# Kernel tuning notes

Hardware: AMD Instinct MI355X
Metric: run time of the kernel (lower is better)

Reference implementation:

```python
import jax, jax.numpy as jnp
import numpy as np

HIDDEN = 2048
HEADS = 16
HEAD_DIM = HIDDEN // HEADS  # 128
ROPE_BASE = 10000.0


def _rope_cos_sin(seq_len, head_dim, dtype):
    inv_freq = 1.0 / (ROPE_BASE ** (jnp.arange(0, head_dim, 2, dtype=jnp.float32) / head_dim))
    pos = jnp.arange(seq_len, dtype=jnp.float32)
    freqs = pos[:, None] * inv_freq[None, :]            # [S, D/2]
    emb = jnp.concatenate([freqs, freqs], axis=-1)      # [S, D]
    return jnp.cos(emb).astype(dtype), jnp.sin(emb).astype(dtype)


def _rotate_half(x):
    x1, x2 = jnp.split(x, 2, axis=-1)
    return jnp.concatenate([-x2, x1], axis=-1)


def apply_rope(q, k, seq_len):
    # q, k: [B, H, S, Dh]
    cos, sin = _rope_cos_sin(seq_len, q.shape[-1], q.dtype)
    q = q * cos + _rotate_half(q) * sin
    k = k * cos + _rotate_half(k) * sin
    return q, k


def setup_inputs() -> dict:
    key = jax.random.key(0)
    ks = jax.random.split(key, 5)
    B, S = 2, 2048
    scale = 1.0 / np.sqrt(HIDDEN)
    return {
        "hidden_states": jax.random.normal(ks[0], (B, S, HIDDEN), dtype=jnp.float32),
        "w_qkv": jax.random.normal(ks[1], (3 * HIDDEN, HIDDEN), dtype=jnp.float32) * scale,
        "b_qkv": jnp.zeros((3 * HIDDEN,), dtype=jnp.float32),
        "w_dense": jax.random.normal(ks[2], (HIDDEN, HIDDEN), dtype=jnp.float32) * scale,
        "b_dense": jnp.zeros((HIDDEN,), dtype=jnp.float32),
    }


def reference(hidden_states, w_qkv, b_qkv, w_dense, b_dense):
    B, S, _ = hidden_states.shape
    qkv = hidden_states @ w_qkv.T + b_qkv                      # [B, S, 3*H*Dh]
    qkv = qkv.reshape(B, S, 3, HEADS, HEAD_DIM)
    qkv = jnp.transpose(qkv, (2, 0, 3, 1, 4))                  # [3, B, H, S, Dh]
    q, k, v = qkv[0], qkv[1], qkv[2]

    # pos_encoding.apply_to_qk -> RoPE
    q, k = apply_rope(q, k, S)

    scale = HEAD_DIM ** (-0.5)
    scores = jnp.einsum("bhqd,bhkd->bhqk", q, k) * scale       # [B, H, S, S]

    # pos_encoding.apply_to_scores -> causal additive mask
    causal = jnp.tril(jnp.ones((S, S), dtype=bool))
    scores = jnp.where(causal, scores, jnp.finfo(scores.dtype).min)

    attn = jax.nn.softmax(scores, axis=-1)
    out = jnp.einsum("bhqk,bhkd->bhqd", attn, v)               # [B, H, S, Dh]
    out = jnp.transpose(out, (0, 2, 1, 3)).reshape(B, S, HIDDEN)
    return out @ w_dense.T + b_dense
```

## Files before the change

### kernel.cpp

```cpp
#include <hip/hip_runtime.h>
#include <hip/hip_bf16.h>
#include <stdint.h>

#define HID 2048
#define NHEAD 16
#define DHEAD 128
#define BB 2
#define SS 2048
#define MM (BB*SS)
#define NQKV (3*HID)
#define NT (SS/64)

typedef __attribute__((ext_vector_type(8))) short bf16x8;
typedef __attribute__((ext_vector_type(4))) float f32x4;
typedef unsigned short ushort_t;

__device__ __forceinline__ f32x4 mfma16(bf16x8 a, bf16x8 b, f32x4 c) {
    return __builtin_amdgcn_mfma_f32_16x16x32_bf16(a, b, c, 0, 0, 0);
}

__device__ __forceinline__ float bf2f(ushort_t u) {
    unsigned int x = ((unsigned int)u) << 16;
    return __builtin_bit_cast(float, x);
}
__device__ __forceinline__ ushort_t f2bf(float f) {
    unsigned int x = __builtin_bit_cast(unsigned int, f);
    unsigned int r = (x + 0x7FFFu + ((x >> 16) & 1u)) >> 16;
    return (ushort_t)r;
}

__device__ __forceinline__ void cvt8(const float* __restrict__ g, ushort_t* l) {
    float4 a = *(const float4*)g;
    float4 b = *(const float4*)(g + 4);
    union { ushort_t u[8]; uint4 v; } t;
    t.u[0] = f2bf(a.x); t.u[1] = f2bf(a.y); t.u[2] = f2bf(a.z); t.u[3] = f2bf(a.w);
    t.u[4] = f2bf(b.x); t.u[5] = f2bf(b.y); t.u[6] = f2bf(b.z); t.u[7] = f2bf(b.w);
    *(uint4*)l = t.v;
}

__device__ __forceinline__ void gload16(const ushort_t* g, ushort_t* l) {
    __builtin_amdgcn_global_load_lds(
        (const __attribute__((address_space(1))) unsigned int*)(const void*)g,
        (__attribute__((address_space(3))) unsigned int*)(void*)l,
        16, 0, 0);
}

#define WAITV0 asm volatile("s_waitcnt vmcnt(0)" ::: "memory")
#define WAITV4 asm volatile("s_waitcnt vmcnt(4)" ::: "memory")
#define WAITV6 asm volatile("s_waitcnt vmcnt(6)" ::: "memory")
#define WAITV8 asm volatile("s_waitcnt vmcnt(8)" ::: "memory")
#define BAR()  __builtin_amdgcn_s_barrier()

__global__ void cvt3_kernel(const float* __restrict__ a, ushort_t* __restrict__ da, int na,
                            const float* __restrict__ b, ushort_t* __restrict__ db, int nb,
                            const float* __restrict__ c, ushort_t* __restrict__ dc, int nc)
{
    int i = blockIdx.x * blockDim.x + threadIdx.x;
    if (i < na) {
        cvt8(a + (size_t)i * 8, da + (size_t)i * 8);
    } else if (i < na + nb) {
        int j = i - na;
        cvt8(b + (size_t)j * 8, db + (size_t)j * 8);
    } else if (i < na + nb + nc) {
        int j = i - na - nb;
        cvt8(c + (size_t)j * 8, dc + (size_t)j * 8);
    }
}

#define BM 256
#define BN 128
#define BKK 64
#define NTK (HID/BKK)
#define ASZ (BM*BKK)
#define BSZ (BN*BKK)
#define BUFSZ (ASZ+BSZ)

__global__ __launch_bounds__(512, 1) void qkv_gemm_fast(
    const ushort_t* __restrict__ X,
    const ushort_t* __restrict__ W,
    const float* __restrict__ bias,
    ushort_t* __restrict__ qws,
    ushort_t* __restrict__ kws,
    ushort_t* __restrict__ vtws)
{
    __shared__ __align__(16) ushort_t smem[3 * BUFSZ];

    const int tid  = threadIdx.x;
    const int lane = tid & 63;
    const int w    = tid >> 6;
    const int wm   = w >> 1, wn = w & 1;
    const int quad = lane >> 4;
    const int l15  = lane & 15;
    const int sub  = (lane & 7) ^ (lane >> 3);
    const int rloc = lane >> 3;
    const int m0 = blockIdx.y * BM;
    const int n0 = blockIdx.x * BN;
    const bool vmode = (n0 >= 2 * HID);

    const ushort_t* gA = X + (size_t)m0 * HID;
    const ushort_t* gB = W + (size_t)n0 * HID;

    f32x4 acc[4][4];
#pragma unroll
    for (int i = 0; i < 4; i++)
#pragma unroll
        for (int j = 0; j < 4; j++)
#pragma unroll
            for (int e = 0; e < 4; e++) acc[i][j][e] = 0.f;

    auto STAGE = [&](int bufi, int t) {
        ushort_t* lA = smem + bufi * BUFSZ;
        ushort_t* lB = lA + ASZ;
        const ushort_t* ga = gA + t * BKK;
        const ushort_t* gb = gB + t * BKK;
#pragma unroll
        for (int i = 0; i < 4; i++) {
            int blk = w * 4 + i;
            gload16(ga + (size_t)(blk * 8 + rloc) * HID + sub * 8, lA + blk * 512);
        }
#pragma unroll
        for (int i = 0; i < 2; i++) {
            int blk = w * 2 + i;
            gload16(gb + (size_t)(blk * 8 + rloc) * HID + sub * 8, lB + blk * 512);
        }
    };

    auto COMPUTE = [&](int bufi) {
        const ushort_t* lA = smem + bufi * BUFSZ;
        const ushort_t* lB = lA + ASZ;
        bf16x8 af[2][4], bfr[2][4];
#pragma unroll
        for (int kk = 0; kk < 2; kk++) {
            const int cs = ((kk * 4 + quad) ^ (l15 & 7)) << 3;
#pragma unroll
            for (int mb = 0; mb < 4; mb++)
                af[kk][mb] = *(const bf16x8*)(lA + (wm * 64 + mb * 16 + l15) * 64 + cs);
#pragma unroll
            for (int nb = 0; nb < 4; nb++)
                bfr[kk][nb] = *(const bf16x8*)(lB + (wn * 64 + nb * 16 + l15) * 64 + cs);
        }
        __builtin_amdgcn_s_setprio(1);
        if (!vmode) {
#pragma unroll
            for (int kk = 0; kk < 2; kk++)
#pragma unroll
                for (int mb = 0; mb < 4; mb++)
#pragma unroll
                    for (int nb = 0; nb < 4; nb++)
                        acc[mb][nb] = mfma16(af[kk][mb], bfr[kk][nb], acc[mb][nb]);
        } else {
#pragma unroll
            for (int kk = 0; kk < 2; kk++)
#pragma unroll
                for (int mb = 0; mb < 4; mb++)
#pragma unroll
                    for (int nb = 0; nb < 4; nb++)
                        acc[mb][nb] = mfma16(bfr[kk][nb], af[kk][mb], acc[mb][nb]);
        }
        __builtin_amdgcn_s_setprio(0);
    };

    STAGE(0, 0);
    STAGE(1, 1);
    WAITV6;
    BAR();

    int buf = 0;
    for (int t = 0; t < NTK - 2; t++) {
        int b2 = buf + 2; if (b2 >= 3) b2 -= 3;
        STAGE(b2, t + 2);
        COMPUTE(buf);
        WAITV6;
        BAR();
        buf++; if (buf == 3) buf = 0;
    }
    COMPUTE(buf);
    WAITV0;
    BAR();
    buf++; if (buf == 3) buf = 0;
    COMPUTE(buf);

    if (!vmode) {
#pragma unroll
        for (int nb = 0; nb < 4; nb++) {
            int n = n0 + wn * 64 + nb * 16 + l15;
            float bv = bias[n];
            int mat = n >> 11;
            int h   = (n >> 7) & 15;
            int d   = n & 127;
            ushort_t* dst = (mat == 0) ? qws : kws;
#pragma unroll
            for (int mb = 0; mb < 4; mb++) {
#pragma unroll
                for (int r = 0; r < 4; r++) {
                    int m = m0 + wm * 64 + mb * 16 + quad * 4 + r;
                    int b = m >> 11;
                    int s = m & 2047;
                    dst[(((size_t)(b * 16 + h) * SS) + s) * DHEAD + d] =
                        f2bf(acc[mb][nb][r] + bv);
                }
            }
        }
    } else {
        const int b = m0 >> 11;
#pragma unroll
        for (int nb = 0; nb < 4; nb++) {
#pragma unroll
            for (int r = 0; r < 4; r++) {
                int n = n0 + wn * 64 + nb * 16 + quad * 4 + r;
                float bv = bias[n];
                int h = (n >> 7) & 15;
                int d = n & 127;
#pragma unroll
                for (int mb = 0; mb < 4; mb++) {
                    int s = (m0 & 2047) + wm * 64 + mb * 16 + l15;
                    vtws[(((size_t)(b * 16 + h) * DHEAD) + d) * SS + s] =
                        f2bf(acc[mb][nb][r] + bv);
                }
            }
        }
    }
}

__global__ __launch_bounds__(512, 1) void dense_gemm_fast(
    const ushort_t* __restrict__ A,
    const ushort_t* __restrict__ W,
    const float* __restrict__ bias,
    float* __restrict__ out)
{
    __shared__ __align__(16) ushort_t smem[3 * BUFSZ];

    const int tid  = threadIdx.x;
    const int lane = tid & 63;
    const int w    = tid >> 6;
    const int wm   = w >> 1;
    const int wn   = w & 1;
    const int quad = lane >> 4;
    const int l15  = lane & 15;
    const int sub  = (lane & 7) ^ (lane >> 3);
    const int rloc = lane >> 3;
    const int m0 = blockIdx.y * BM;
    const int n0 = blockIdx.x * BN;

    const ushort_t* gA = A + (size_t)m0 * HID;
    const ushort_t* gB = W + (size_t)n0 * HID;

    f32x4 acc[4][4];
#pragma unroll
    for (int i = 0; i < 4; i++)
#pragma unroll
        for (int j = 0; j < 4; j++)
#pragma unroll
            for (int e = 0; e < 4; e++) acc[i][j][e] = 0.f;

    auto STAGE = [&](int bufi, int t) {
        ushort_t* lA = smem + bufi * BUFSZ;
        ushort_t* lB = lA + ASZ;
        const ushort_t* ga = gA + t * BKK;
        const ushort_t* gb = gB + t * BKK;
#pragma unroll
        for (int i = 0; i < 4; i++) {
            int blk = w * 4 + i;
            gload16(ga + (size_t)(blk * 8 + rloc) * HID + sub * 8, lA + blk * 512);
        }
#pragma unroll
        for (int i = 0; i < 2; i++) {
            int blk = w * 2 + i;
            gload16(gb + (size_t)(blk * 8 + rloc) * HID + sub * 8, lB + blk * 512);
        }
    };

    auto COMPUTE = [&](int bufi) {
        const ushort_t* lA = smem + bufi * BUFSZ;
        const ushort_t* lB = lA + ASZ;
        bf16x8 af[2][4], bfr[2][4];
#pragma unroll
        for (int kk = 0; kk < 2; kk++) {
            const int cs = ((kk * 4 + quad) ^ (l15 & 7)) << 3;
#pragma unroll
            for (int mb = 0; mb < 4; mb++)
                af[kk][mb] = *(const bf16x8*)(lA + (wm * 64 + mb * 16 + l15) * 64 + cs);
#pragma unroll
            for (int nb = 0; nb < 4; nb++)
                bfr[kk][nb] = *(const bf16x8*)(lB + (wn * 64 + nb * 16 + l15) * 64 + cs);
        }
        __builtin_amdgcn_s_setprio(1);
#pragma unroll
        for (int kk = 0; kk < 2; kk++)
#pragma unroll
            for (int mb = 0; mb < 4; mb++)
#pragma unroll
                for (int nb = 0; nb < 4; nb++)
                    acc[mb][nb] = mfma16(af[kk][mb], bfr[kk][nb], acc[mb][nb]);
        __builtin_amdgcn_s_setprio(0);
    };

    STAGE(0, 0);
    STAGE(1, 1);
    WAITV6;
    BAR();

    int buf = 0;
    for (int t = 0; t < NTK - 2; t++) {
        int b2 = buf + 2; if (b2 >= 3) b2 -= 3;
        STAGE(b2, t + 2);
        COMPUTE(buf);
        WAITV6;
        BAR();
        buf++; if (buf == 3) buf = 0;
    }
    COMPUTE(buf);
    WAITV0;
    BAR();
    buf++; if (buf == 3) buf = 0;
    COMPUTE(buf);

#pragma unroll
    for (int nb = 0; nb < 4; nb++) {
        int n = n0 + wn * 64 + nb * 16 + l15;
        float bv = bias[n];
#pragma unroll
        for (int mb = 0; mb < 4; mb++) {
#pragma unroll
            for (int r = 0; r < 4; r++) {
                int m = m0 + wm * 64 + mb * 16 + quad * 4 + r;
                out[(size_t)m * HID + n] = acc[mb][nb][r] + bv;
            }
        }
    }
}

__global__ void rope_kernel3(ushort_t* __restrict__ qws, ushort_t* __restrict__ kws)
{
    int t = blockIdx.x * blockDim.x + threadIdx.x;
    int d2g = t & 7;
    int s   = (t >> 3) & 2047;
    int bh0 = (t >> 14) * 4;

    float sn[8], cs[8];
#pragma unroll
    for (int jj = 0; jj < 8; jj++) {
        int d2 = d2g * 8 + jj;
        float inv_freq = exp2f(-(float)d2 * (13.287712379549449f / 64.f));
        float fr = (float)s * inv_freq;
        sincosf(fr, &sn[jj], &cs[jj]);
    }

    size_t base0 = (size_t)s * DHEAD + d2g * 8;
#pragma unroll
    for (int q = 0; q < 4; q++) {
        size_t base = base0 + (size_t)(bh0 + q) * (SS * DHEAD);
        {
            union { ushort_t u[8]; uint4 v; } x1, x2, y1, y2;
            x1.v = *(const uint4*)(qws + base);
            x2.v = *(const uint4*)(qws + base + 64);
#pragma unroll
            for (int jj = 0; jj < 8; jj++) {
                float a = bf2f(x1.u[jj]), b = bf2f(x2.u[jj]);
                y1.u[jj] = f2bf(a * cs[jj] - b * sn[jj]);
                y2.u[jj] = f2bf(b * cs[jj] + a * sn[jj]);
            }
            *(uint4*)(qws + base) = y1.v;
            *(uint4*)(qws + base + 64) = y2.v;
        }
        {
            union { ushort_t u[8]; uint4 v; } x1, x2, y1, y2;
            x1.v = *(const uint4*)(kws + base);
            x2.v = *(const uint4*)(kws + base + 64);
#pragma unroll
            for (int jj = 0; jj < 8; jj++) {
                float a = bf2f(x1.u[jj]), b = bf2f(x2.u[jj]);
                y1.u[jj] = f2bf(a * cs[jj] - b * sn[jj]);
                y2.u[jj] = f2bf(b * cs[jj] + a * sn[jj]);
            }
            *(uint4*)(kws + base) = y1.v;
            *(uint4*)(kws + base + 64) = y2.v;
        }
    }
}

#define LDP 72

__global__ __launch_bounds__(256, 2) void attn_kernel5(
    const ushort_t* __restrict__ qws,
    const ushort_t* __restrict__ kws,
    const ushort_t* __restrict__ vtws,
    ushort_t* __restrict__ aout)
{
    __shared__ __align__(16) ushort_t k_s[2][64 * 128];
    __shared__ __align__(16) ushort_t vt_s[128 * 64];
    __shared__ __align__(16) ushort_t pA_s[4][16 * LDP];
    __shared__ __align__(16) ushort_t pB_s[4][16 * LDP];

    const int tid  = threadIdx.x;
    const int lane = tid & 63;
    const int w    = tid >> 6;
    const int quad = lane >> 4;
    const int l15  = lane & 15;

    const int g  = blockIdx.x;
    const int bh = (g & 7) | (((g >> 3) & 3) << 3);
    const int tA = g >> 5;
    const int tB = NT - 1 - tA;
    const int qA = tA * 64, qB = tB * 64;
    const size_t qk_base = (size_t)bh * SS * DHEAD;

    bf16x8 qa[4], qb[4];
    {
        const ushort_t* rowA = qws + qk_base + (size_t)(qA + w * 16 + l15) * DHEAD;
        const ushort_t* rowB = qws + qk_base + (size_t)(qB + w * 16 + l15) * DHEAD;
#pragma unroll
        for (int kc = 0; kc < 4; kc++) {
            qa[kc] = *(const bf16x8*)(rowA + kc * 32 + quad * 8);
            qb[kc] = *(const bf16x8*)(rowB + kc * 32 + quad * 8);
        }
    }

    bf16x8 ones;
#pragma unroll
    for (int i = 0; i < 8; i++) ones[i] = (short)0x3F80;

    f32x4 oA[8], oB[8], lA, lB;
#pragma unroll
    for (int i = 0; i < 8; i++)
#pragma unroll
        for (int e = 0; e < 4; e++) { oA[i][e] = 0.f; oB[i][e] = 0.f; }
#pragma unroll
    for (int e = 0; e < 4; e++) { lA[e] = 0.f; lB[e] = 0.f; }

    const int srowK = lane >> 4;
    const int srowV = lane >> 3;
    const int ccgV  = (lane & 7) ^ (lane >> 3);

    const int q_baseA = qA + w * 16 + quad * 4;
    const int q_baseB = qB + w * 16 + quad * 4;
    const int xorv = l15 & 7;

    const float scale2 = 0.12753102015727466f;
    const float FM = 16.0f;

    auto KSTAGE = [&](int j, int slot) {
        const int kb = j * 64;
#pragma unroll
        for (int i = 0; i < 4; i++) {
            int P = i * 4 + w;
            int row = P * 4 + srowK;
            int ccg = l15 ^ (((P & 1) * 4) + srowK);
            gload16(kws + qk_base + (size_t)(kb + row) * DHEAD + ccg * 8,
                    k_s[slot] + P * 512);
        }
    };
    auto VSTAGE = [&](int j) {
        const int kb = j * 64;
#pragma unroll
        for (int i = 0; i < 4; i++) {
            int P = i * 4 + w;
            int row = P * 8 + srowV;
            gload16(vtws + qk_base + (size_t)row * SS + kb + ccgV * 8,
                    vt_s + P * 512);
        }
    };

    KSTAGE(0, 0);

    for (int j = 0; j <= tB; j++) {
        const int kb = j * 64;
        const int slot = j & 1;

        VSTAGE(j);
        if (j < tB) {
            KSTAGE(j + 1, slot ^ 1);
            WAITV8;
        } else {
            WAITV4;
        }
        BAR();

        f32x4 sA[4], sB[4];
#pragma unroll
        for (int nb = 0; nb < 4; nb++)
#pragma unroll
            for (int e = 0; e < 4; e++) { sA[nb][e] = 0.f; sB[nb][e] = 0.f; }

        const ushort_t* ks = k_s[slot];

        if (j <= tA) {
#pragma unroll
            for (int kc = 0; kc < 4; kc++) {
#pragma unroll
                for (int nb = 0; nb < 4; nb++) {
                    int cc_s = (kc * 4 + quad) ^ xorv;
                    bf16x8 kf = *(const bf16x8*)(ks + (nb * 16 + l15) * 128 + cc_s * 8);
                    sA[nb] = mfma16(qa[kc], kf, sA[nb]);
                    sB[nb] = mfma16(qb[kc], kf, sB[nb]);
                }
            }
#pragma unroll
            for (int nb = 0; nb < 4; nb++) {
                int kidx = kb + nb * 16 + l15;
#pragma unroll
                for (int r = 0; r < 4; r++) {
                    float pa = exp2f(sA[nb][r] * scale2 - FM);
                    float pb = exp2f(sB[nb][r] * scale2 - FM);
                    pa = (kidx <= q_baseA + r) ? pa : 0.f;
                    pb = (kidx <= q_baseB + r) ? pb : 0.f;
                    pA_s[w][(quad * 4 + r) * LDP + nb * 16 + l15] = f2bf(pa);
                    pB_s[w][(quad * 4 + r) * LDP + nb * 16 + l15] = f2bf(pb);
                }
            }
            if (j < tB) { WAITV4; } else { WAITV0; }
            BAR();
#pragma unroll
            for (int kc = 0; kc < 2; kc++) {
                bf16x8 pa = *(const bf16x8*)(pA_s[w] + l15 * LDP + kc * 32 + quad * 8);
                bf16x8 pb = *(const bf16x8*)(pB_s[w] + l15 * LDP + kc * 32 + quad * 8);
                lA = mfma16(pa, ones, lA);
                lB = mfma16(pb, ones, lB);
#pragma unroll
                for (int db = 0; db < 8; db++) {
                    int cc_s = (kc * 4 + quad) ^ xorv;
                    bf16x8 vf = *(const bf16x8*)(vt_s + (db * 16 + l15) * 64 + cc_s * 8);
                    oA[db] = mfma16(pa, vf, oA[db]);
                    oB[db] = mfma16(pb, vf, oB[db]);
                }
            }
        } else {
#pragma unroll
            for (int kc = 0; kc < 4; kc++) {
#pragma unroll
                for (int nb = 0; nb < 4; nb++) {
                    int cc_s = (kc * 4 + quad) ^ xorv;
                    bf16x8 kf = *(const bf16x8*)(ks + (nb * 16 + l15) * 128 + cc_s * 8);
                    sB[nb] = mfma16(qb[kc], kf, sB[nb]);
                }
            }
#pragma unroll
            for (int nb = 0; nb < 4; nb++) {
                int kidx = kb + nb * 16 + l15;
#pragma unroll
                for (int r = 0; r < 4; r++) {
                    float pb = exp2f(sB[nb][r] * scale2 - FM);
                    pb = (kidx <= q_baseB + r) ? pb : 0.f;
                    pB_s[w][(quad * 4 + r) * LDP + nb * 16 + l15] = f2bf(pb);
                }
            }
            if (j < tB) { WAITV4; } else { WAITV0; }
            BAR();
#pragma unroll
            for (int kc = 0; kc < 2; kc++) {
                bf16x8 pb = *(const bf16x8*)(pB_s[w] + l15 * LDP + kc * 32 + quad * 8);
                lB = mfma16(pb, ones, lB);
#pragma unroll
                for (int db = 0; db < 8; db++) {
                    int cc_s = (kc * 4 + quad) ^ xorv;
                    bf16x8 vf = *(const bf16x8*)(vt_s + (db * 16 + l15) * 64 + cc_s * 8);
                    oB[db] = mfma16(pb, vf, oB[db]);
                }
            }
        }
        BAR();
    }

    const int b = bh >> 4;
    const int h = bh & 15;
    float invA[4], invB[4];
#pragma unroll
    for (int r = 0; r < 4; r++) { invA[r] = 1.f / lA[r]; invB[r] = 1.f / lB[r]; }
#pragma unroll
    for (int db = 0; db < 8; db++) {
#pragma unroll
        for (int r = 0; r < 4; r++) {
            int sA_row = qA + w * 16 + quad * 4 + r;
            int sB_row = qB + w * 16 + quad * 4 + r;
            size_t offA = ((size_t)(b * SS + sA_row)) * HID + h * DHEAD + db * 16 + l15;
            size_t offB = ((size_t)(b * SS + sB_row)) * HID + h * DHEAD + db * 16 + l15;
            aout[offA] = f2bf(oA[db][r] * invA[r]);
            aout[offB] = f2bf(oB[db][r] * invB[r]);
        }
    }
}

extern "C" void kernel_launch(void* const* d_in, const int* in_sizes, int n_in,
                              void* d_out, int out_size, void* d_ws, size_t ws_size,
                              hipStream_t stream)
{
    const float* X    = (const float*)d_in[0];
    const float* Wqkv = (const float*)d_in[1];
    const float* bqkv = (const float*)d_in[2];
    const float* Wd   = (const float*)d_in[3];
    const float* bd   = (const float*)d_in[4];
    float* out = (float*)d_out;

    char* ws = (char*)d_ws;
    const size_t MB = 1048576;
    ushort_t* qws  = (ushort_t*)(ws);
    ushort_t* kws  = (ushort_t*)(ws + 16 * MB);
    ushort_t* vtws = (ushort_t*)(ws + 32 * MB);
    ushort_t* aout = (ushort_t*)(ws + 48 * MB);
    ushort_t* Xbf  = (ushort_t*)(ws + 48 * MB);
    ushort_t* Wqbf = (ushort_t*)(ws + 64 * MB);
    ushort_t* Wdbf = (ushort_t*)(ws + 88 * MB);

    const int nX = MM * HID / 8, nWq = NQKV * HID / 8, nWd = HID * HID / 8;
    cvt3_kernel<<<(nX + nWq + nWd + 255) / 256, 256, 0, stream>>>(
        X, Xbf, nX, Wqkv, Wqbf, nWq, Wd, Wdbf, nWd);

    qkv_gemm_fast<<<dim3(NQKV / BN, MM / BM), 512, 0, stream>>>(Xbf, Wqbf, bqkv, qws, kws, vtws);
    rope_kernel3<<<(SS * 8 * 8) / 256, 256, 0, stream>>>(qws, kws);
    attn_kernel5<<<dim3(NT / 2 * BB * NHEAD), 256, 0, stream>>>(qws, kws, vtws, aout);
    dense_gemm_fast<<<dim3(HID / BN, MM / BM), 512, 0, stream>>>(aout, Wdbf, bd, out);
}
```

Before: 375.3 us.

## Enlarge attention query tile to 128 rows with 8 waves and double-buffered V

The attention kernel now uses 512-thread blocks with eight waves, each block handling a pair of 128-row query tiles instead of 64-row ones. Each K/V tile loaded into LDS is therefore reused by twice as many query rows, which cuts global K/V traffic. The V tile is now double-buffered like K so its load can overlap with compute, and the vmcnt waits are adjusted to match. The cost is fewer blocks (256), one block per CU, more LDS per block and less scheduling flexibility for load balance.

```diff
diff --git a/kernel.cpp b/kernel.cpp
--- a/kernel.cpp
+++ b/kernel.cpp
@@ -9,7 +9,6 @@
 #define SS 2048
 #define MM (BB*SS)
 #define NQKV (3*HID)
-#define NT (SS/64)
 
 typedef __attribute__((ext_vector_type(8))) short bf16x8;
 typedef __attribute__((ext_vector_type(4))) float f32x4;
@@ -46,9 +45,9 @@
 }
 
 #define WAITV0 asm volatile("s_waitcnt vmcnt(0)" ::: "memory")
+#define WAITV2 asm volatile("s_waitcnt vmcnt(2)" ::: "memory")
 #define WAITV4 asm volatile("s_waitcnt vmcnt(4)" ::: "memory")
 #define WAITV6 asm volatile("s_waitcnt vmcnt(6)" ::: "memory")
-#define WAITV8 asm volatile("s_waitcnt vmcnt(8)" ::: "memory")
 #define BAR()  __builtin_amdgcn_s_barrier()
 
 __global__ void cvt3_kernel(const float* __restrict__ a, ushort_t* __restrict__ da, int na,
@@ -381,16 +380,16 @@
 
 #define LDP 72
 
-__global__ __launch_bounds__(256, 2) void attn_kernel5(
+__global__ __launch_bounds__(512, 1) void attn_kernel6(
     const ushort_t* __restrict__ qws,
     const ushort_t* __restrict__ kws,
     const ushort_t* __restrict__ vtws,
     ushort_t* __restrict__ aout)
 {
     __shared__ __align__(16) ushort_t k_s[2][64 * 128];
-    __shared__ __align__(16) ushort_t vt_s[128 * 64];
-    __shared__ __align__(16) ushort_t pA_s[4][16 * LDP];
-    __shared__ __align__(16) ushort_t pB_s[4][16 * LDP];
+    __shared__ __align__(16) ushort_t vt_s[2][128 * 64];
+    __shared__ __align__(16) ushort_t pA_s[8][16 * LDP];
+    __shared__ __align__(16) ushort_t pB_s[8][16 * LDP];
 
     const int tid  = threadIdx.x;
     const int lane = tid & 63;
@@ -401,8 +400,10 @@
     const int g  = blockIdx.x;
     const int bh = (g & 7) | (((g >> 3) & 3) << 3);
     const int tA = g >> 5;
-    const int tB = NT - 1 - tA;
-    const int qA = tA * 64, qB = tB * 64;
+    const int tB = 15 - tA;
+    const int qA = tA * 128, qB = tB * 128;
+    const int jAmax = 2 * tA + 1;
+    const int jBmax = 2 * tB + 1;
     const size_t qk_base = (size_t)bh * SS * DHEAD;
 
     bf16x8 qa[4], qb[4];
@@ -442,37 +443,37 @@
     auto KSTAGE = [&](int j, int slot) {
         const int kb = j * 64;
 #pragma unroll
-        for (int i = 0; i < 4; i++) {
-            int P = i * 4 + w;
+        for (int i = 0; i < 2; i++) {
+            int P = i * 8 + w;
             int row = P * 4 + srowK;
             int ccg = l15 ^ (((P & 1) * 4) + srowK);
             gload16(kws + qk_base + (size_t)(kb + row) * DHEAD + ccg * 8,
                     k_s[slot] + P * 512);
         }
     };
-    auto VSTAGE = [&](int j) {
+    auto VSTAGE = [&](int j, int slot) {
         const int kb = j * 64;
 #pragma unroll
-        for (int i = 0; i < 4; i++) {
-            int P = i * 4 + w;
+        for (int i = 0; i < 2; i++) {
+            int P = i * 8 + w;
             int row = P * 8 + srowV;
             gload16(vtws + qk_base + (size_t)row * SS + kb + ccgV * 8,
-                    vt_s + P * 512);
+                    vt_s[slot] + P * 512);
         }
     };
 
     KSTAGE(0, 0);
 
-    for (int j = 0; j <= tB; j++) {
+    for (int j = 0; j <= jBmax; j++) {
         const int kb = j * 64;
         const int slot = j & 1;
 
-        VSTAGE(j);
-        if (j < tB) {
+        VSTAGE(j, slot);
+        if (j < jBmax) {
             KSTAGE(j + 1, slot ^ 1);
-            WAITV8;
+            WAITV4;
         } else {
-            WAITV4;
+            WAITV2;
         }
         BAR();
 
@@ -483,8 +484,9 @@
             for (int e = 0; e < 4; e++) { sA[nb][e] = 0.f; sB[nb][e] = 0.f; }
 
         const ushort_t* ks = k_s[slot];
-
-        if (j <= tA) {
+        const ushort_t* vs = vt_s[slot];
+
+        if (j <= jAmax) {
 #pragma unroll
             for (int kc = 0; kc < 4; kc++) {
 #pragma unroll
@@ -508,7 +510,7 @@
                     pB_s[w][(quad * 4 + r) * LDP + nb * 16 + l15] = f2bf(pb);
                 }
             }
-            if (j < tB) { WAITV4; } else { WAITV0; }
+            if (j < jBmax) { WAITV2; } else { WAITV0; }
             BAR();
 #pragma unroll
             for (int kc = 0; kc < 2; kc++) {
@@ -519,7 +521,7 @@
 #pragma unroll
                 for (int db = 0; db < 8; db++) {
                     int cc_s = (kc * 4 + quad) ^ xorv;
-                    bf16x8 vf = *(const bf16x8*)(vt_s + (db * 16 + l15) * 64 + cc_s * 8);
+                    bf16x8 vf = *(const bf16x8*)(vs + (db * 16 + l15) * 64 + cc_s * 8);
                     oA[db] = mfma16(pa, vf, oA[db]);
                     oB[db] = mfma16(pb, vf, oB[db]);
                 }
@@ -544,7 +546,7 @@
                     pB_s[w][(quad * 4 + r) * LDP + nb * 16 + l15] = f2bf(pb);
                 }
             }
-            if (j < tB) { WAITV4; } else { WAITV0; }
+            if (j < jBmax) { WAITV2; } else { WAITV0; }
             BAR();
 #pragma unroll
             for (int kc = 0; kc < 2; kc++) {
@@ -553,7 +555,7 @@
 #pragma unroll
                 for (int db = 0; db < 8; db++) {
                     int cc_s = (kc * 4 + quad) ^ xorv;
-                    bf16x8 vf = *(const bf16x8*)(vt_s + (db * 16 + l15) * 64 + cc_s * 8);
+                    bf16x8 vf = *(const bf16x8*)(vs + (db * 16 + l15) * 64 + cc_s * 8);
                     oB[db] = mfma16(pb, vf, oB[db]);
                 }
             }
@@ -607,6 +609,6 @@
 
     qkv_gemm_fast<<<dim3(NQKV / BN, MM / BM), 512, 0, stream>>>(Xbf, Wqbf, bqkv, qws, kws, vtws);
     rope_kernel3<<<(SS * 8 * 8) / 256, 256, 0, stream>>>(qws, kws);
-    attn_kernel5<<<dim3(NT / 2 * BB * NHEAD), 256, 0, stream>>>(qws, kws, vtws, aout);
+    attn_kernel6<<<dim3(256), 512, 0, stream>>>(qws, kws, vtws, aout);
     dense_gemm_fast<<<dim3(HID / BN, MM / BM), 512, 0, stream>>>(aout, Wdbf, bd, out);
 }
```

New measurement: 386.4 us. 1.03x slower.
